# Kernel optimization log

Measured on AMD Instinct MI355X. Metric: run time of the kernel, lower is better.

The kernel has to match this reference:

```python
import jax, jax.numpy as jnp
import numpy as np

B, S, NH, HD = 2, 2048, 32, 128     # batch seqs, tokens per seq, heads, head_dim
H = NH * HD                          # hidden = 4096
BLOCK = 64                           # paged KV-cache block size
NBLK = S // BLOCK                    # blocks per sequence
NUM_BLOCKS = B * NBLK                # total cache blocks


def alibi_slopes(n):
    # n is a power of two: slope_i = 2^(-8*(i+1)/n)
    return np.asarray([2.0 ** (-8.0 * (i + 1) / n) for i in range(n)], dtype=np.float32)


def setup_inputs() -> dict:
    key = jax.random.key(0)
    k1, k2, k3 = jax.random.split(key, 3)
    hidden_states = jax.random.normal(k1, (B * S, H), jnp.float32)
    w_pack = jax.random.normal(k2, (H, 3 * H), jnp.float32) * 0.02
    o_proj_w = jax.random.normal(k3, (H, H), jnp.float32) * 0.02
    k_cache = jnp.zeros((NUM_BLOCKS, BLOCK, NH, HD), jnp.float32)
    v_cache = jnp.zeros((NUM_BLOCKS, BLOCK, NH, HD), jnp.float32)
    block_offsets = jnp.arange(NUM_BLOCKS, dtype=jnp.int32).reshape(B, NBLK)
    return {
        "hidden_states": hidden_states,
        "w_pack": w_pack,
        "o_proj_w": o_proj_w,
        "k_cache": k_cache,
        "v_cache": v_cache,
        "block_offsets": block_offsets,
    }


def reference(hidden_states, w_pack, o_proj_w, k_cache, v_cache, block_offsets):
    # fused QKV projection, chunk(3, -1)
    qkv = hidden_states @ w_pack                      # [B*S, 3H]
    q, k, v = jnp.split(qkv, 3, axis=-1)
    q = q.reshape(B, S, NH, HD)
    k = k.reshape(B, NBLK, BLOCK, NH, HD)
    v = v.reshape(B, NBLK, BLOCK, NH, HD)

    # fill_kv_cache: scatter new K/V into paged cache blocks
    k_cache = k_cache.at[block_offsets].set(k)        # [NUM_BLOCKS, BLOCK, NH, HD]
    v_cache = v_cache.at[block_offsets].set(v)

    # paged read: gather non-contiguous blocks back per sequence
    kg = k_cache[block_offsets].reshape(B, S, NH, HD)
    vg = v_cache[block_offsets].reshape(B, S, NH, HD)

    slopes = jnp.asarray(alibi_slopes(NH))            # [NH]
    scale = 1.0 / jnp.sqrt(jnp.float32(HD))
    scores = jnp.einsum('bqhd,bkhd->bhqk', q, kg) * scale   # [B,NH,S,S]
    pos = jnp.arange(S)
    # ALiBi bias: slope * key_position (row-shift invariant under softmax)
    scores = scores + slopes[None, :, None, None] * pos[None, None, None, :]
    causal = pos[:, None] >= pos[None, :]             # [S,S]
    scores = jnp.where(causal[None, None], scores, jnp.float32(-1e30))
    probs = jax.nn.softmax(scores, axis=-1)
    attn = jnp.einsum('bhqk,bkhd->bqhd', probs, vg).reshape(B * S, H)
    return attn @ o_proj_w
```

## Files before the change

### kernel.cpp

```cpp
#include <hip/hip_runtime.h>
#include <hip/hip_bf16.h>
#include <stdint.h>

typedef __attribute__((ext_vector_type(4))) float f32x4;
typedef __attribute__((ext_vector_type(8))) __bf16 bf16x8;
typedef __attribute__((ext_vector_type(8))) unsigned short u16x8;
typedef __attribute__((ext_vector_type(4))) unsigned short u16x4;
typedef __attribute__((ext_vector_type(2))) unsigned int u32x2;
typedef __attribute__((ext_vector_type(4))) unsigned int u32x4;

#define GLL16(g, l) __builtin_amdgcn_global_load_lds( \
    (const __attribute__((address_space(1))) unsigned int*)(uintptr_t)(g), \
    (__attribute__((address_space(3))) unsigned int*)(uintptr_t)(l), 16, 0, 0)

__device__ __forceinline__ unsigned short bf16u(float f) {
  return __builtin_bit_cast(unsigned short, __float2bfloat16(f));
}

#define PB 2
#define PS 2048
#define PNH 32
#define PHD 128
#define PH 4096
#define P3H 12288

__global__ __launch_bounds__(256)
void cvt_f32_bf16(const float* __restrict__ in, unsigned short* __restrict__ out, int n) {
  int stride = gridDim.x * blockDim.x;
  for (int i = blockIdx.x * blockDim.x + threadIdx.x; i * 8 < n; i += stride) {
    int base = i * 8;
    f32x4 a = *(const f32x4*)(in + base);
    f32x4 b = *(const f32x4*)(in + base + 4);
    u16x8 o;
#pragma unroll
    for (int j = 0; j < 4; ++j) { o[j] = bf16u(a[j]); o[4 + j] = bf16u(b[j]); }
    *(u16x8*)(out + base) = o;
  }
}

__global__ __launch_bounds__(256)
void transpose_cvt(const float* __restrict__ in, unsigned short* __restrict__ out,
                   int K, int N) {
  __shared__ __align__(16) unsigned short tile[64][68];
  int k0 = blockIdx.y * 64, n0 = blockIdx.x * 64;
  int t = threadIdx.x;
  int rr = t >> 4, cc = (t & 15) * 4;
#pragma unroll
  for (int p = 0; p < 4; ++p) {
    int r = rr + p * 16;
    f32x4 v = *(const f32x4*)(in + (size_t)(k0 + r) * N + n0 + cc);
    u16x4 w;
#pragma unroll
    for (int j = 0; j < 4; ++j) w[j] = bf16u(v[j]);
    *(u16x4*)&tile[r][cc] = w;
  }
  __syncthreads();
#pragma unroll
  for (int p = 0; p < 4; ++p) {
    int nl = rr + p * 16;
    u16x4 w;
#pragma unroll
    for (int j = 0; j < 4; ++j) w[j] = tile[cc + j][nl];
    *(u16x4*)(out + (size_t)(n0 + nl) * K + k0 + cc) = w;
  }
}

#define STAGE_A(TT) do { int sb_ = ((TT) & 3) << 15; \
    GLL16(aSrc0 + (size_t)(TT) * 32, smem + sb_ + (wave << 10)); \
    GLL16(aSrc1 + (size_t)(TT) * 32, smem + sb_ + 8192 + (wave << 10)); } while (0)
#define STAGE_B(TT) do { int sb_ = ((TT) & 3) << 15; \
    GLL16(bSrc0 + (size_t)(TT) * 32, smem + sb_ + 16384 + (wave << 10)); \
    GLL16(bSrc1 + (size_t)(TT) * 32, smem + sb_ + 24576 + (wave << 10)); } while (0)

#define TILEBODY(T, DOSTAGE, VM) do { \
    char* AsB_ = smem + (((T) & 3) << 15); \
    char* BsB_ = AsB_ + 16384; \
    if (DOSTAGE) { STAGE_A((T) + 2); STAGE_B((T) + 2); } \
    bf16x8 av[8], bv[4]; \
    _Pragma("unroll") \
    for (int i = 0; i < 8; ++i) \
      av[i] = *(const bf16x8*)(AsB_ + (((wm << 7) + (i << 4) + lr) << 6) + lchunk); \
    _Pragma("unroll") \
    for (int j = 0; j < 4; ++j) \
      bv[j] = *(const bf16x8*)(BsB_ + (((wn << 6) + (j << 4) + lr) << 6) + lchunk); \
    if ((VM) == 4)      asm volatile("s_waitcnt vmcnt(4)" ::: "memory"); \
    else if ((VM) == 0) asm volatile("s_waitcnt vmcnt(0)" ::: "memory"); \
    __builtin_amdgcn_s_barrier(); \
    __builtin_amdgcn_s_setprio(1); \
    _Pragma("unroll") \
    for (int i = 0; i < 8; ++i) \
      _Pragma("unroll") \
      for (int j = 0; j < 4; ++j) \
        acc[i][j] = __builtin_amdgcn_mfma_f32_16x16x32_bf16(av[i], bv[j], acc[i][j], 0, 0, 0); \
    __builtin_amdgcn_s_setprio(0); \
  } while (0)

template<int OUTF32>
__global__ __launch_bounds__(512, 2)
void gemm256(const unsigned short* __restrict__ A, const unsigned short* __restrict__ Bt,
             void* __restrict__ Cv, int M, int N, int K) {
  __shared__ __align__(16) char smem[131072];
  const int tid = threadIdx.x;
  const int wave = tid >> 6, lane = tid & 63;
  const int lr = lane & 15, lg = lane >> 4;
  const int wm = wave >> 2, wn = wave & 3;
  const int lchunk = (lg ^ ((lr >> 1) & 3)) << 4;
  const int nbn = N >> 8;
  const int nwg = (M >> 8) * nbn;
  int bid = blockIdx.x;
  int qq = nwg >> 3;
  int wg = (bid & 7) * qq + (bid >> 3);
  int bm = wg / nbn, bn = wg % nbn;
  const size_t arow = (size_t)bm << 8;
  const size_t brow = (size_t)bn << 8;

  const int srow = (wave << 4) + (lane >> 2);
  const int scol = ((lane & 3) ^ ((lane >> 3) & 3)) << 3;
  const unsigned short* aSrc0 = A  + (arow + srow) * K + scol;
  const unsigned short* aSrc1 = A  + (arow + 128 + srow) * K + scol;
  const unsigned short* bSrc0 = Bt + (brow + srow) * K + scol;
  const unsigned short* bSrc1 = Bt + (brow + 128 + srow) * K + scol;

  f32x4 acc[8][4] = {};

  STAGE_A(0); STAGE_B(0); STAGE_A(1); STAGE_B(1);
  asm volatile("s_waitcnt vmcnt(4)" ::: "memory");
  __builtin_amdgcn_s_barrier();

  const int NT = K >> 5;
  for (int t = 0; t < NT - 2; ++t) TILEBODY(t, 1, 4);
  TILEBODY(NT - 2, 0, 0);
  TILEBODY(NT - 1, 0, -1);

  int crow = (bm << 8) + (wm << 7) + (lg << 2);
  int ccol = (bn << 8) + (wn << 6) + lr;
#pragma unroll
  for (int i = 0; i < 8; ++i)
#pragma unroll
    for (int j = 0; j < 4; ++j)
#pragma unroll
      for (int r = 0; r < 4; ++r) {
        size_t off = (size_t)(crow + (i << 4) + r) * N + ccol + (j << 4);
        if (OUTF32) ((float*)Cv)[off] = acc[i][j][r];
        else        ((unsigned short*)Cv)[off] = bf16u(acc[i][j][r]);
      }
}

__global__ __launch_bounds__(256, 2)
void attn_kernel(const unsigned short* __restrict__ qkv, unsigned short* __restrict__ out) {
  __shared__ __align__(16) unsigned short Ks[2][64 * 128];
  __shared__ __align__(16) unsigned short Vt[128 * 64];
  __shared__ __align__(16) unsigned short Ps[4][32 * 88];
  int tid = threadIdx.x, wave = tid >> 6, lane = tid & 63;
  int lr = lane & 15, lg = lane >> 4;
  int idx = blockIdx.x;
  int qt = 15 - (idx & 15);
  int h = (idx >> 4) & 31, b = idx >> 9;
  size_t rb = (size_t)b * PS;
  int qcol = h << 7, kcol = PH + (h << 7), vcol = 2 * PH + (h << 7);
  int q0 = (qt << 7) + (wave << 5);

  bf16x8 aq[2][4];
#pragma unroll
  for (int qs = 0; qs < 2; ++qs)
#pragma unroll
    for (int f = 0; f < 4; ++f)
      aq[qs][f] = *(const bf16x8*)(qkv + (rb + q0 + (qs << 4) + lr) * P3H + qcol + (f << 5) + (lg << 3));

  float m_run[2][4], l_run[2][4];
#pragma unroll
  for (int qs = 0; qs < 2; ++qs)
#pragma unroll
    for (int r = 0; r < 4; ++r) { m_run[qs][r] = -1e30f; l_run[qs][r] = 0.f; }
  f32x4 acc_o[2][8] = {};

  float slope2 = __builtin_amdgcn_exp2f(-(float)(h + 1) * 0.25f) * 1.44269504f;
  const float scale2 = 0.08838834764831845f * 1.44269504f;

  char* KsB = (char*)Ks;
  char* VtB = (char*)Vt;
  const int kk0 = (tid & 15) << 2, d0 = (tid >> 4) << 3;

  {
    size_t krow = rb;
#pragma unroll
    for (int i = 0; i < 4; ++i) {
      int pf = (wave << 12) | (i << 10) | (lane << 4);
      int row = pf >> 8;
      int lch = ((pf >> 4) & 15) ^ (row & 7);
      GLL16(qkv + (krow + row) * P3H + kcol + (lch << 3), KsB + (wave << 12) + (i << 10));
    }
  }
  u32x4 vr0 = *(const u32x4*)(qkv + (rb + kk0 + 0) * P3H + vcol + d0);
  u32x4 vr1 = *(const u32x4*)(qkv + (rb + kk0 + 1) * P3H + vcol + d0);
  u32x4 vr2 = *(const u32x4*)(qkv + (rb + kk0 + 2) * P3H + vcol + d0);
  u32x4 vr3 = *(const u32x4*)(qkv + (rb + kk0 + 3) * P3H + vcol + d0);

  const int tmax = 2 * qt + 1;
  for (int t = 0; t <= tmax; ++t) {
    int cur = t & 1;
    char* KsCur = KsB + (cur << 14);
    char* KsNxt = KsB + ((cur ^ 1) << 14);
    bool more = (t < tmax);

    u32x4 nv0 = {}, nv1 = {}, nv2 = {}, nv3 = {};
    if (more) {
      size_t krow = rb + ((size_t)(t + 1) << 6);
#pragma unroll
      for (int i = 0; i < 4; ++i) {
        int pf = (wave << 12) | (i << 10) | (lane << 4);
        int row = pf >> 8;
        int lch = ((pf >> 4) & 15) ^ (row & 7);
        GLL16(qkv + (krow + row) * P3H + kcol + (lch << 3), KsNxt + (wave << 12) + (i << 10));
      }
      nv0 = *(const u32x4*)(qkv + (krow + kk0 + 0) * P3H + vcol + d0);
      nv1 = *(const u32x4*)(qkv + (krow + kk0 + 1) * P3H + vcol + d0);
      nv2 = *(const u32x4*)(qkv + (krow + kk0 + 2) * P3H + vcol + d0);
      nv3 = *(const u32x4*)(qkv + (krow + kk0 + 3) * P3H + vcol + d0);
    }

    if (more) asm volatile("s_waitcnt vmcnt(8)" ::: "memory");
    else      asm volatile("s_waitcnt vmcnt(0)" ::: "memory");

    {
      const unsigned short* e0 = (const unsigned short*)&vr0;
      const unsigned short* e1 = (const unsigned short*)&vr1;
      const unsigned short* e2 = (const unsigned short*)&vr2;
      const unsigned short* e3 = (const unsigned short*)&vr3;
#pragma unroll
      for (int j = 0; j < 8; ++j) {
        int d = d0 + j;
        u32x2 w;
        w.x = (unsigned int)e0[j] | ((unsigned int)e1[j] << 16);
        w.y = (unsigned int)e2[j] | ((unsigned int)e3[j] << 16);
        int byteoff = ((d << 7) + (kk0 << 1)) ^ ((d & 7) << 4);
        *(u32x2*)(VtB + byteoff) = w;
      }
    }
    asm volatile("s_waitcnt lgkmcnt(0)" ::: "memory");
    __builtin_amdgcn_s_barrier();

    f32x4 sc[2][4];
    __builtin_amdgcn_s_setprio(1);
#pragma unroll
    for (int f = 0; f < 4; ++f) {
      f32x4 c0 = {}, c1 = {};
#pragma unroll
      for (int ks = 0; ks < 4; ++ks) {
        int kkr = (f << 4) + lr;
        int ch = (lg + (ks << 2)) ^ (kkr & 7);
        bf16x8 bk = *(const bf16x8*)(KsCur + (kkr << 8) + (ch << 4));
        c0 = __builtin_amdgcn_mfma_f32_16x16x32_bf16(aq[0][ks], bk, c0, 0, 0, 0);
        c1 = __builtin_amdgcn_mfma_f32_16x16x32_bf16(aq[1][ks], bk, c1, 0, 0, 0);
      }
      sc[0][f] = c0; sc[1][f] = c1;
    }
    __builtin_amdgcn_s_setprio(0);

    int kvb = t << 6;
    bool needmask = (kvb + 63 > q0);
#pragma unroll
    for (int qs = 0; qs < 2; ++qs) {
      float vals[4][4];
#pragma unroll
      for (int f = 0; f < 4; ++f) {
        int kv = kvb + (f << 4) + lr;
        float bias = slope2 * (float)kv;
#pragma unroll
        for (int r = 0; r < 4; ++r) {
          float v = sc[qs][f][r] * scale2 + bias;
          if (needmask && kv > q0 + (qs << 4) + (lg << 2) + r) v = -1e30f;
          vals[r][f] = v;
        }
      }
      float alpha[4];
#pragma unroll
      for (int r = 0; r < 4; ++r) {
        float mr = fmaxf(fmaxf(vals[r][0], vals[r][1]), fmaxf(vals[r][2], vals[r][3]));
#pragma unroll
        for (int d2 = 1; d2 < 16; d2 <<= 1) mr = fmaxf(mr, __shfl_xor(mr, d2, 16));
        float mnew = fmaxf(m_run[qs][r], mr);
        alpha[r] = __builtin_amdgcn_exp2f(m_run[qs][r] - mnew);
        m_run[qs][r] = mnew;
      }
#pragma unroll
      for (int r = 0; r < 4; ++r) {
        float s = 0.f;
#pragma unroll
        for (int f = 0; f < 4; ++f) {
          float p = __builtin_amdgcn_exp2f(vals[r][f] - m_run[qs][r]);
          s += p;
          Ps[wave][((qs << 4) + (lg << 2) + r) * 88 + (f << 4) + lr] = bf16u(p);
        }
        l_run[qs][r] = l_run[qs][r] * alpha[r] + s;
      }
#pragma unroll
      for (int d = 0; d < 8; ++d) {
        f32x4 a4 = acc_o[qs][d];
#pragma unroll
        for (int r = 0; r < 4; ++r) a4[r] *= alpha[r];
        acc_o[qs][d] = a4;
      }
    }

    bf16x8 pa[2][2];
#pragma unroll
    for (int qs = 0; qs < 2; ++qs)
#pragma unroll
      for (int ks = 0; ks < 2; ++ks)
        pa[qs][ks] = *(const bf16x8*)((char*)&Ps[wave][0] + ((qs << 4) + lr) * 176 + (ks << 6) + (lg << 4));
    __builtin_amdgcn_s_setprio(1);
#pragma unroll
    for (int d = 0; d < 8; ++d) {
#pragma unroll
      for (int ks = 0; ks < 2; ++ks) {
        int dr = (d << 4) + lr;
        int ch = (lg + (ks << 2)) ^ (dr & 7);
        bf16x8 bv = *(const bf16x8*)(VtB + (dr << 7) + (ch << 4));
        acc_o[0][d] = __builtin_amdgcn_mfma_f32_16x16x32_bf16(pa[0][ks], bv, acc_o[0][d], 0, 0, 0);
        acc_o[1][d] = __builtin_amdgcn_mfma_f32_16x16x32_bf16(pa[1][ks], bv, acc_o[1][d], 0, 0, 0);
      }
    }
    __builtin_amdgcn_s_setprio(0);
    __builtin_amdgcn_s_barrier();

    if (more) { vr0 = nv0; vr1 = nv1; vr2 = nv2; vr3 = nv3; }
  }

#pragma unroll
  for (int qs = 0; qs < 2; ++qs) {
    float rinv[4];
#pragma unroll
    for (int r = 0; r < 4; ++r) {
      float s = l_run[qs][r];
#pragma unroll
      for (int d2 = 1; d2 < 16; d2 <<= 1) s += __shfl_xor(s, d2, 16);
      rinv[r] = 1.f / s;
    }
#pragma unroll
    for (int d = 0; d < 8; ++d)
#pragma unroll
      for (int r = 0; r < 4; ++r) {
        float o = acc_o[qs][d][r] * rinv[r];
        out[(rb + q0 + (qs << 4) + (lg << 2) + r) * PH + (h << 7) + (d << 4) + lr] = bf16u(o);
      }
  }
}

extern "C" void kernel_launch(void* const* d_in, const int* in_sizes, int n_in,
                              void* d_out, int out_size, void* d_ws, size_t ws_size,
                              hipStream_t stream) {
  const float* hidden = (const float*)d_in[0];
  const float* w_pack = (const float*)d_in[1];
  const float* o_proj = (const float*)d_in[2];

  char* ws = (char*)d_ws;
  unsigned short* wpackT = (unsigned short*)(ws);
  unsigned short* qkv    = (unsigned short*)(ws + 100663296);
  unsigned short* oprojT = (unsigned short*)(ws + 201326592);
  unsigned short* hbf    = (unsigned short*)(ws + 234881024);
  unsigned short* attnb  = hbf;

  int M = PB * PS;

  cvt_f32_bf16<<<2048, 256, 0, stream>>>(hidden, hbf, M * PH);
  transpose_cvt<<<dim3(P3H / 64, PH / 64), 256, 0, stream>>>(w_pack, wpackT, PH, P3H);
  transpose_cvt<<<dim3(PH / 64, PH / 64), 256, 0, stream>>>(o_proj, oprojT, PH, PH);
  gemm256<0><<<(M / 256) * (P3H / 256), 512, 0, stream>>>(hbf, wpackT, qkv, M, P3H, PH);
  attn_kernel<<<PB * PNH * (PS / 128), 256, 0, stream>>>(qkv, attnb);
  gemm256<1><<<(M / 256) * (PH / 256), 512, 0, stream>>>(attnb, oprojT, d_out, M, PH, PH);
}
```

Baseline: 858.7 us.

## Software-pipeline GEMM mainloop with register double-buffering and interleaved LDS reads

Rewrites the bf16 GEMM mainloop so the LDS fragment reads for the next K-tile are interleaved with the current tile's MFMAs. A fragments are double-buffered in registers (avA/avB) and sched_group_barrier is used to interleave the work. Global-to-LDS prefetch is deepened from 2 to 3 tiles ahead across the 4 LDS buffers, with one load slice issued per MFMA group. The aim is to hide LDS latency and the barrier stall before each MFMA burst, at the cost of more registers and a loop hardcoded to 128 K-tiles (K=4096).

```diff
diff --git a/kernel.cpp b/kernel.cpp
--- a/kernel.cpp
+++ b/kernel.cpp
@@ -65,34 +65,34 @@
   }
 }
 
-#define STAGE_A(TT) do { int sb_ = ((TT) & 3) << 15; \
-    GLL16(aSrc0 + (size_t)(TT) * 32, smem + sb_ + (wave << 10)); \
-    GLL16(aSrc1 + (size_t)(TT) * 32, smem + sb_ + 8192 + (wave << 10)); } while (0)
-#define STAGE_B(TT) do { int sb_ = ((TT) & 3) << 15; \
-    GLL16(bSrc0 + (size_t)(TT) * 32, smem + sb_ + 16384 + (wave << 10)); \
-    GLL16(bSrc1 + (size_t)(TT) * 32, smem + sb_ + 24576 + (wave << 10)); } while (0)
-
-#define TILEBODY(T, DOSTAGE, VM) do { \
-    char* AsB_ = smem + (((T) & 3) << 15); \
-    char* BsB_ = AsB_ + 16384; \
-    if (DOSTAGE) { STAGE_A((T) + 2); STAGE_B((T) + 2); } \
-    bf16x8 av[8], bv[4]; \
+#define GLLP(TT, P) do { int sb_ = ((TT) & 3) << 15; \
+    const unsigned short* s_ = (P) == 0 ? aSrc0 : (P) == 1 ? aSrc1 : (P) == 2 ? bSrc0 : bSrc1; \
+    GLL16(s_ + (size_t)(TT) * 32, smem + sb_ + ((P) << 13) + (wave << 10)); } while (0)
+
+#define RD_AV(DST, BUFP, I) DST[I] = *(const bf16x8*)((BUFP) + (((wm << 7) + ((I) << 4) + lr) << 6) + lchunk)
+#define RD_BV(DST, BUFP, J) DST[J] = *(const bf16x8*)((BUFP) + 16384 + (((wn << 6) + ((J) << 4) + lr) << 6) + lchunk)
+
+#define SGB __builtin_amdgcn_sched_group_barrier
+
+#define TILE(TC, AC, AN, DOSTAGE, DOREAD, VM, DOBAR) do { \
+    char* nA_ = smem + ((((TC) + 1) & 3) << 15); \
+    __builtin_amdgcn_s_setprio(1); \
     _Pragma("unroll") \
-    for (int i = 0; i < 8; ++i) \
-      av[i] = *(const bf16x8*)(AsB_ + (((wm << 7) + (i << 4) + lr) << 6) + lchunk); \
-    _Pragma("unroll") \
-    for (int j = 0; j < 4; ++j) \
-      bv[j] = *(const bf16x8*)(BsB_ + (((wn << 6) + (j << 4) + lr) << 6) + lchunk); \
+    for (int g = 0; g < 4; ++g) { \
+      if (DOREAD) { RD_AV(AN, nA_, 2 * g); RD_AV(AN, nA_, 2 * g + 1); } \
+      if (DOSTAGE) GLLP((TC) + 3, g); \
+      _Pragma("unroll") \
+      for (int i = 2 * g; i < 2 * g + 2; ++i) \
+        _Pragma("unroll") \
+        for (int j = 0; j < 4; ++j) \
+          acc[i][j] = __builtin_amdgcn_mfma_f32_16x16x32_bf16(AC[i], bvv[j], acc[i][j], 0, 0, 0); \
+      SGB(0x100, 2, 0); SGB(0x020, 1, 0); SGB(0x008, 8, 0); \
+    } \
+    if (DOREAD) { RD_BV(bvv, nA_, 0); RD_BV(bvv, nA_, 1); RD_BV(bvv, nA_, 2); RD_BV(bvv, nA_, 3); } \
+    __builtin_amdgcn_s_setprio(0); \
     if ((VM) == 4)      asm volatile("s_waitcnt vmcnt(4)" ::: "memory"); \
     else if ((VM) == 0) asm volatile("s_waitcnt vmcnt(0)" ::: "memory"); \
-    __builtin_amdgcn_s_barrier(); \
-    __builtin_amdgcn_s_setprio(1); \
-    _Pragma("unroll") \
-    for (int i = 0; i < 8; ++i) \
-      _Pragma("unroll") \
-      for (int j = 0; j < 4; ++j) \
-        acc[i][j] = __builtin_amdgcn_mfma_f32_16x16x32_bf16(av[i], bv[j], acc[i][j], 0, 0, 0); \
-    __builtin_amdgcn_s_setprio(0); \
+    if (DOBAR) __builtin_amdgcn_s_barrier(); \
   } while (0)
 
 template<int OUTF32>
@@ -123,14 +123,33 @@
 
   f32x4 acc[8][4] = {};
 
-  STAGE_A(0); STAGE_B(0); STAGE_A(1); STAGE_B(1);
+#pragma unroll
+  for (int p = 0; p < 4; ++p) GLLP(0, p);
+#pragma unroll
+  for (int p = 0; p < 4; ++p) GLLP(1, p);
+#pragma unroll
+  for (int p = 0; p < 4; ++p) GLLP(2, p);
   asm volatile("s_waitcnt vmcnt(4)" ::: "memory");
   __builtin_amdgcn_s_barrier();
 
-  const int NT = K >> 5;
-  for (int t = 0; t < NT - 2; ++t) TILEBODY(t, 1, 4);
-  TILEBODY(NT - 2, 0, 0);
-  TILEBODY(NT - 1, 0, -1);
+  bf16x8 avA[8], avB[8], bvv[4];
+  {
+    char* b0 = smem;
+#pragma unroll
+    for (int i = 0; i < 8; ++i) RD_AV(avA, b0, i);
+#pragma unroll
+    for (int j = 0; j < 4; ++j) RD_BV(bvv, b0, j);
+  }
+
+  for (int p = 0; p < 62; ++p) {
+    int t = 2 * p;
+    TILE(t,     avA, avB, 1, 1, 4, 1);
+    TILE(t + 1, avB, avA, 1, 1, 4, 1);
+  }
+  TILE(124, avA, avB, 1, 1, 4, 1);
+  TILE(125, avB, avA, 0, 1, 0, 1);
+  TILE(126, avA, avB, 0, 1, -1, 0);
+  TILE(127, avB, avA, 0, 0, -1, 0);
 
   int crow = (bm << 8) + (wm << 7) + (lg << 2);
   int ccol = (bn << 8) + (wn << 6) + lr;
```

Measured after the change: 850.5 us. No clear change (-0.9%).
